# Optimization experiments

Hardware: AMD Instinct MI355X
Metric: run time of the kernel (lower is better)

The kernel has to match this reference:

```python
import jax, jax.numpy as jnp
import numpy as np

D_MODEL = 1024
H = 16
D_K = D_MODEL // H
NEG = -1e9


def setup_inputs() -> dict:
    key = jax.random.key(0)
    ks = jax.random.split(key, 8)
    B, S = 4, 2048
    q = jax.random.normal(ks[0], (B, S, D_MODEL), dtype=jnp.float32)
    k = jax.random.normal(ks[1], (B, S, D_MODEL), dtype=jnp.float32)
    v = jax.random.normal(ks[2], (B, S, D_MODEL), dtype=jnp.float32)
    mask = jax.random.randint(ks[3], (B, S), 0, 2, dtype=jnp.int32)
    scale = 1.0 / np.sqrt(D_MODEL)
    Wq = jax.random.normal(ks[4], (D_MODEL, D_MODEL), dtype=jnp.float32) * scale
    Wk = jax.random.normal(ks[5], (D_MODEL, D_MODEL), dtype=jnp.float32) * scale
    Wv = jax.random.normal(ks[6], (D_MODEL, D_MODEL), dtype=jnp.float32) * scale
    Wo = jax.random.normal(ks[7], (D_MODEL, D_MODEL), dtype=jnp.float32) * scale
    return {"q": q, "k": k, "v": v, "mask": mask,
            "Wq": Wq, "Wk": Wk, "Wv": Wv, "Wo": Wo}


def _split_heads(x):
    # [B,S,d_model] -> [B,H,S,d_k]
    B, S, _ = x.shape
    return x.reshape(B, S, H, D_K).transpose(0, 2, 1, 3)


def reference(q, k, v, mask, Wq, Wk, Wv, Wo):
    # Linear projections (torch Linear: x @ W.T, no bias)
    query = _split_heads(jnp.einsum('bsd,ed->bse', q, Wq))
    key_ = _split_heads(jnp.einsum('bsd,ed->bse', k, Wk))
    value = _split_heads(jnp.einsum('bsd,ed->bse', v, Wv))
    # scaled dot-product attention, manual path
    scores = jnp.einsum('bhqd,bhkd->bhqk', query, key_) / jnp.sqrt(
        jnp.asarray(D_K, dtype=query.dtype))
    m = (mask == 0)[:, None, None, :]  # [B,1,1,S]
    scores = jnp.where(m, jnp.asarray(NEG, dtype=scores.dtype), scores)
    attn = jax.nn.softmax(scores, axis=-1)
    mh = jnp.einsum('bhqk,bhkd->bhqd', attn, value)
    # merge heads -> [B,S,d_model]
    B = mh.shape[0]
    mh = mh.transpose(0, 2, 1, 3).reshape(B, -1, D_MODEL)
    return jnp.einsum('bsd,ed->bse', mh, Wo)
```

## Files before the change

### kernel.cpp

```cpp
#include <hip/hip_runtime.h>

typedef __attribute__((ext_vector_type(4))) float f32x4;
typedef __attribute__((ext_vector_type(8))) __bf16 bf16x8;
typedef __attribute__((ext_vector_type(2))) __bf16 bf16x2;

#if defined(__has_builtin)
#if __has_builtin(__builtin_amdgcn_exp2f)
#define EXP2F(x) __builtin_amdgcn_exp2f(x)
#endif
#if __has_builtin(__builtin_amdgcn_cvt_pk_bf16_f32)
#define HAVE_CVT_PK 1
#endif
#endif
#ifndef EXP2F
#define EXP2F(x) __builtin_exp2f(x)
#endif

__device__ __forceinline__ ushort f2bf(float f) {
  unsigned int u = __float_as_uint(f);
  return (ushort)((u + 0x7FFFu + ((u >> 16) & 1u)) >> 16);
}

__device__ __forceinline__ uint pack_bf16(float a, float b) {
#ifdef HAVE_CVT_PK
  bf16x2 p = __builtin_amdgcn_cvt_pk_bf16_f32(a, b);
  return __builtin_bit_cast(uint, p);
#else
  return (uint)f2bf(a) | ((uint)f2bf(b) << 16);
#endif
}

__device__ __forceinline__ void async_cp16(const void* g, void* l) {
  __builtin_amdgcn_global_load_lds(
      (const __attribute__((address_space(1))) void*)g,
      (__attribute__((address_space(3))) void*)l, 16, 0, 0);
}


__global__ __launch_bounds__(256) void cast_bf16_kernel(const float* __restrict__ in,
                                                        ushort* __restrict__ out, int n4) {
  int i = blockIdx.x * 256 + threadIdx.x;
  if (i < n4) {
    float4 f = ((const float4*)in)[i];
    uint2 o;
    o.x = pack_bf16(f.x, f.y);
    o.y = pack_bf16(f.z, f.w);
    ((uint2*)out)[i] = o;
  }
}

__global__ __launch_bounds__(256) void cast3_kernel(const float* __restrict__ q,
                                                    const float* __restrict__ k,
                                                    const float* __restrict__ v,
                                                    ushort* qo, ushort* ko, ushort* vo) {
  int y = blockIdx.y;
  const float* in = y == 0 ? q : (y == 1 ? k : v);
  ushort* out = y == 0 ? qo : (y == 1 ? ko : vo);
  int i = blockIdx.x * 256 + threadIdx.x;
  float4 f = ((const float4*)in)[i];
  uint2 o;
  o.x = pack_bf16(f.x, f.y);
  o.y = pack_bf16(f.z, f.w);
  ((uint2*)out)[i] = o;
}

__global__ __launch_bounds__(256) void cast4_kernel(const float* __restrict__ a,
                                                    const float* __restrict__ b,
                                                    const float* __restrict__ c,
                                                    const float* __restrict__ d,
                                                    ushort* ao, ushort* bo, ushort* co, ushort* do_) {
  int y = blockIdx.y;
  const float* in = y == 0 ? a : (y == 1 ? b : (y == 2 ? c : d));
  ushort* out = y == 0 ? ao : (y == 1 ? bo : (y == 2 ? co : do_));
  int i = blockIdx.x * 256 + threadIdx.x;
  float4 f = ((const float4*)in)[i];
  uint2 o;
  o.x = pack_bf16(f.x, f.y);
  o.y = pack_bf16(f.z, f.w);
  ((uint2*)out)[i] = o;
}


__device__ __forceinline__ void gemm_body(const ushort* __restrict__ A,
                                          const ushort* __restrict__ W,
                                          void* __restrict__ Cout, int mode) {
  constexpr int N = 1024, K = 1024;
  __shared__ ushort As[128 * 32];
  __shared__ ushort Bs[128 * 32];
  const int bm = blockIdx.y * 128;
  const int bn = blockIdx.x * 128;
  const int tid = threadIdx.x;
  const int w = tid >> 6, lane = tid & 63;
  const int g = lane >> 4, cc = lane & 15;
  const int wm = (w >> 1) * 64, wn = (w & 1) * 64;

  f32x4 acc[4][4];
#pragma unroll
  for (int i = 0; i < 4; ++i)
#pragma unroll
    for (int j = 0; j < 4; ++j) acc[i][j] = (f32x4)0.0f;

  for (int k0 = 0; k0 < K; k0 += 32) {
#pragma unroll
    for (int j = 0; j < 2; ++j) {
      int cbase = w * 128 + j * 64;
      int cid = cbase + lane;
      int row = cid & 127, kb = cid >> 7;
      async_cp16(A + (size_t)(bm + row) * K + k0 + kb * 8, &As[cbase * 8]);
      async_cp16(W + (size_t)(bn + row) * K + k0 + kb * 8, &Bs[cbase * 8]);
    }
    __syncthreads();
    bf16x8 af[4], bfr[4];
#pragma unroll
    for (int mi = 0; mi < 4; ++mi)
      af[mi] = *(const bf16x8*)&As[(g * 128 + wm + mi * 16 + cc) * 8];
#pragma unroll
    for (int ni = 0; ni < 4; ++ni)
      bfr[ni] = *(const bf16x8*)&Bs[(g * 128 + wn + ni * 16 + cc) * 8];
#pragma unroll
    for (int mi = 0; mi < 4; ++mi)
#pragma unroll
      for (int ni = 0; ni < 4; ++ni)
        acc[mi][ni] = __builtin_amdgcn_mfma_f32_16x16x32_bf16(af[mi], bfr[ni], acc[mi][ni], 0, 0, 0);
    __syncthreads();
  }

#pragma unroll
  for (int mi = 0; mi < 4; ++mi) {
#pragma unroll
    for (int ni = 0; ni < 4; ++ni) {
#pragma unroll
      for (int r = 0; r < 4; ++r) {
        int row = bm + wm + mi * 16 + g * 4 + r;
        int col = bn + wn + ni * 16 + cc;
        float val = acc[mi][ni][r];
        if (mode == 0) {
          ((ushort*)Cout)[(size_t)row * N + col] = f2bf(val);
        } else if (mode == 1) {
          ((float*)Cout)[(size_t)row * N + col] = val;
        } else {
          int b = row >> 11, s = row & 2047;
          int h = col >> 6, d = col & 63;
          ((ushort*)Cout)[(size_t)((b * 16 + h) * 64 + d) * 2048 + s] = f2bf(val);
        }
      }
    }
  }
}

__global__ __launch_bounds__(256) void qkv_gemm_kernel(const ushort* qb, const ushort* kb,
                                                       const ushort* vb, const ushort* wq,
                                                       const ushort* wk, const ushort* wv,
                                                       ushort* Qp, ushort* Kp, ushort* Vt) {
  int z = blockIdx.z;
  const ushort* A = z == 0 ? qb : (z == 1 ? kb : vb);
  const ushort* W = z == 0 ? wq : (z == 1 ? wk : wv);
  void* C = z == 0 ? (void*)Qp : (z == 1 ? (void*)Kp : (void*)Vt);
  gemm_body(A, W, C, z == 2 ? 2 : 0);
}

__global__ __launch_bounds__(256) void gemm1_kernel(const ushort* A, const ushort* W,
                                                    void* C, int mode) {
  gemm_body(A, W, C, mode);
}

__global__ __launch_bounds__(256, 4) void attn_kernel(const ushort* __restrict__ Qp,
                                                      const ushort* __restrict__ Kp,
                                                      const ushort* __restrict__ Vt,
                                                      const int* __restrict__ mask,
                                                      ushort* __restrict__ mh) {
  constexpr int S = 2048, DM = 1024, DK = 64;
  __shared__ ushort k_lds[64 * 64];
  __shared__ ushort v_lds[64 * 64];
  __shared__ ushort pt_lds[4 * 2176];

  const int bh = blockIdx.x;
  const int qt = blockIdx.y;
  const int b = bh >> 4, h = bh & 15;
  const int tid = threadIdx.x;
  const int w = tid >> 6, lane = tid & 63;
  const int g = lane >> 4, cc = lane & 15;
  ushort* ptw = &pt_lds[w * 2176];

  const int q0 = qt * 128 + w * 32;
  bf16x8 qf[2][2];
#pragma unroll
  for (int ni = 0; ni < 2; ++ni) {
    size_t row = (size_t)(b * S + q0 + ni * 16 + cc);
#pragma unroll
    for (int ks = 0; ks < 2; ++ks)
      qf[ks][ni] = *(const bf16x8*)&Qp[row * DM + h * DK + ks * 32 + g * 8];
  }

  f32x4 o_acc[4][2];
#pragma unroll
  for (int i = 0; i < 4; ++i)
#pragma unroll
    for (int j = 0; j < 2; ++j) o_acc[i][j] = (f32x4)0.0f;
  float m_i[2] = {-3e38f, -3e38f};
  float l_p[2] = {0.0f, 0.0f};
  const int* maskb = mask + b * S;
  const float csc = 0.18033688011112042f;

  for (int kt = 0; kt < S / 64; ++kt) {
    if (kt) __syncthreads();
#pragma unroll
    for (int j = 0; j < 2; ++j) {
      int cb = j * 256 + w * 64;
      int cid = cb + lane;
      async_cp16(Kp + (size_t)(b * S + kt * 64 + (cid & 63)) * DM + h * DK + (cid >> 6) * 8,
                 &k_lds[cb * 8]);
      async_cp16(Vt + (size_t)(bh * DK + (cid & 63)) * S + kt * 64 + (cid >> 6) * 8,
                 &v_lds[cb * 8]);
    }
    __syncthreads();

    f32x4 sacc[4][2];
#pragma unroll
    for (int mi = 0; mi < 4; ++mi)
#pragma unroll
      for (int ni = 0; ni < 2; ++ni) sacc[mi][ni] = (f32x4)0.0f;
#pragma unroll
    for (int ks = 0; ks < 2; ++ks)
#pragma unroll
      for (int mi = 0; mi < 4; ++mi) {
        bf16x8 kf = *(const bf16x8*)&k_lds[((ks * 4 + g) * 64 + mi * 16 + cc) * 8];
        sacc[mi][0] = __builtin_amdgcn_mfma_f32_16x16x32_bf16(kf, qf[ks][0], sacc[mi][0], 0, 0, 0);
        sacc[mi][1] = __builtin_amdgcn_mfma_f32_16x16x32_bf16(kf, qf[ks][1], sacc[mi][1], 0, 0, 0);
      }

    float mx[2] = {-3e38f, -3e38f};
#pragma unroll
    for (int mi = 0; mi < 4; ++mi) {
      int4 mv = *(const int4*)&maskb[kt * 64 + mi * 16 + g * 4];
      const int* mvp = &mv.x;
#pragma unroll
      for (int r = 0; r < 4; ++r) {
        bool keep = mvp[r] != 0;
#pragma unroll
        for (int ni = 0; ni < 2; ++ni) {
          float t = sacc[mi][ni][r] * csc;
          t = keep ? t : -1e9f;
          sacc[mi][ni][r] = t;
          mx[ni] = fmaxf(mx[ni], t);
        }
      }
    }
    float mn[2];
#pragma unroll
    for (int ni = 0; ni < 2; ++ni) {
      float m = mx[ni];
      m = fmaxf(m, __shfl_xor(m, 16, 64));
      m = fmaxf(m, __shfl_xor(m, 32, 64));
      mn[ni] = fmaxf(m_i[ni], m);
      float al = EXP2F(m_i[ni] - mn[ni]);
      m_i[ni] = mn[ni];
      l_p[ni] *= al;
#pragma unroll
      for (int md = 0; md < 4; ++md)
#pragma unroll
        for (int r = 0; r < 4; ++r) o_acc[md][ni][r] *= al;
    }

#pragma unroll
    for (int mi = 0; mi < 4; ++mi)
#pragma unroll
      for (int ni = 0; ni < 2; ++ni) {
        float p0 = EXP2F(sacc[mi][ni][0] - mn[ni]);
        float p1 = EXP2F(sacc[mi][ni][1] - mn[ni]);
        float p2 = EXP2F(sacc[mi][ni][2] - mn[ni]);
        float p3 = EXP2F(sacc[mi][ni][3] - mn[ni]);
        l_p[ni] += (p0 + p1) + (p2 + p3);
        int base = ((mi * 2 + (g >> 1)) * 32 + ni * 16 + cc) * 8 + (g & 1) * 4;
        *(uint*)&ptw[base] = pack_bf16(p0, p1);
        *(uint*)&ptw[base + 2] = pack_bf16(p2, p3);
      }

#pragma unroll
    for (int ks = 0; ks < 2; ++ks) {
      bf16x8 ptf[2];
#pragma unroll
      for (int ni = 0; ni < 2; ++ni)
        ptf[ni] = *(const bf16x8*)&ptw[((ks * 4 + g) * 32 + ni * 16 + cc) * 8];
#pragma unroll
      for (int md = 0; md < 4; ++md) {
        bf16x8 vf = *(const bf16x8*)&v_lds[((ks * 4 + g) * 64 + md * 16 + cc) * 8];
        o_acc[md][0] = __builtin_amdgcn_mfma_f32_16x16x32_bf16(vf, ptf[0], o_acc[md][0], 0, 0, 0);
        o_acc[md][1] = __builtin_amdgcn_mfma_f32_16x16x32_bf16(vf, ptf[1], o_acc[md][1], 0, 0, 0);
      }
    }
  }

  float rl[2];
#pragma unroll
  for (int ni = 0; ni < 2; ++ni) {
    float l = l_p[ni];
    l += __shfl_xor(l, 16, 64);
    l += __shfl_xor(l, 32, 64);
    rl[ni] = 1.0f / l;
  }
#pragma unroll
  for (int md = 0; md < 4; ++md)
#pragma unroll
    for (int ni = 0; ni < 2; ++ni) {
      int ql = ni * 16 + cc;
      int dbase = md * 16 + g * 4;
      *(uint*)&ptw[ql * 68 + dbase] =
          pack_bf16(o_acc[md][ni][0] * rl[ni], o_acc[md][ni][1] * rl[ni]);
      *(uint*)&ptw[ql * 68 + dbase + 2] =
          pack_bf16(o_acc[md][ni][2] * rl[ni], o_acc[md][ni][3] * rl[ni]);
    }
#pragma unroll
  for (int pass = 0; pass < 4; ++pass) {
    int ql = pass * 8 + (lane >> 3);
    int dc = lane & 7;
    uint4 val = *(const uint4*)&ptw[ql * 68 + dc * 8];
    *(uint4*)&mh[(size_t)(b * S + q0 + ql) * DM + h * DK + dc * 8] = val;
  }
}


extern "C" void kernel_launch(void* const* d_in, const int* in_sizes, int n_in,
                              void* d_out, int out_size, void* d_ws, size_t ws_size,
                              hipStream_t stream) {
  const float* q = (const float*)d_in[0];
  const float* k = (const float*)d_in[1];
  const float* v = (const float*)d_in[2];
  const int* mask = (const int*)d_in[3];
  const float* Wq = (const float*)d_in[4];
  const float* Wk = (const float*)d_in[5];
  const float* Wv = (const float*)d_in[6];
  const float* Wo = (const float*)d_in[7];

  const int M = 8192, Dm = 1024;
  const size_t MB = 1 << 20;

  char* ws = (char*)d_ws;
  ushort* Qp = (ushort*)(ws);
  ushort* Kp = (ushort*)(ws + 16 * MB);
  ushort* Vt = (ushort*)(ws + 32 * MB);
  ushort* wqb = (ushort*)(ws + 48 * MB);
  ushort* wkb = wqb + (1 << 20);
  ushort* wvb = wkb + (1 << 20);
  ushort* wob = wvb + (1 << 20);
  ushort* inbase = (ushort*)(ws + 56 * MB);

  dim3 blk(256);
  dim3 ggrid(Dm / 128, M / 128);

  cast4_kernel<<<dim3(1024, 4), blk, 0, stream>>>(Wq, Wk, Wv, Wo, wqb, wkb, wvb, wob);

  ushort* mh;
  if (ws_size >= 104 * MB) {
    ushort* qb = inbase;
    ushort* kb = inbase + 8 * MB;
    ushort* vb = inbase + 16 * MB;
    cast3_kernel<<<dim3(8192, 3), blk, 0, stream>>>(q, k, v, qb, kb, vb);
    qkv_gemm_kernel<<<dim3(Dm / 128, M / 128, 3), blk, 0, stream>>>(qb, kb, vb, wqb, wkb, wvb,
                                                                    Qp, Kp, Vt);
    mh = qb;
  } else {
    ushort* bufA = inbase;
    cast_bf16_kernel<<<dim3(8192), blk, 0, stream>>>(q, bufA, M * Dm / 4);
    gemm1_kernel<<<ggrid, blk, 0, stream>>>(bufA, wqb, (void*)Qp, 0);
    cast_bf16_kernel<<<dim3(8192), blk, 0, stream>>>(k, bufA, M * Dm / 4);
    gemm1_kernel<<<ggrid, blk, 0, stream>>>(bufA, wkb, (void*)Kp, 0);
    cast_bf16_kernel<<<dim3(8192), blk, 0, stream>>>(v, bufA, M * Dm / 4);
    gemm1_kernel<<<ggrid, blk, 0, stream>>>(bufA, wvb, (void*)Vt, 2);
    mh = bufA;
  }

  attn_kernel<<<dim3(64, 16), blk, 0, stream>>>(Qp, Kp, Vt, mask, mh);
  gemm1_kernel<<<ggrid, blk, 0, stream>>>(mh, wob, d_out, 1);
}
```

Measured before the change: 459.5 us.

## Fold softmax scale into Q projection, precompute mask bias, MFMA row sums

```diff
diff --git a/kernel.cpp b/kernel.cpp
--- a/kernel.cpp
+++ b/kernel.cpp
@@ -1,30 +1,32 @@
 #include <hip/hip_runtime.h>
+#include <math.h>
 
 typedef __attribute__((ext_vector_type(4))) float f32x4;
 typedef __attribute__((ext_vector_type(8))) __bf16 bf16x8;
 typedef __attribute__((ext_vector_type(2))) __bf16 bf16x2;
 
-#if defined(__has_builtin)
+#ifndef __has_builtin
+#define __has_builtin(x) 0
+#endif
+
 #if __has_builtin(__builtin_amdgcn_exp2f)
 #define EXP2F(x) __builtin_amdgcn_exp2f(x)
+#else
+#define EXP2F(x) exp2f(x)
 #endif
+
+__device__ __forceinline__ ushort f2bf(float f) {
+  return (ushort)((__float_as_uint(f) + 0x8000u) >> 16);
+}
+
+__device__ __forceinline__ uint pack_bf16(float a, float b) {
 #if __has_builtin(__builtin_amdgcn_cvt_pk_bf16_f32)
-#define HAVE_CVT_PK 1
-#endif
-#endif
-#ifndef EXP2F
-#define EXP2F(x) __builtin_exp2f(x)
-#endif
-
-__device__ __forceinline__ ushort f2bf(float f) {
-  unsigned int u = __float_as_uint(f);
-  return (ushort)((u + 0x7FFFu + ((u >> 16) & 1u)) >> 16);
-}
-
-__device__ __forceinline__ uint pack_bf16(float a, float b) {
-#ifdef HAVE_CVT_PK
   bf16x2 p = __builtin_amdgcn_cvt_pk_bf16_f32(a, b);
   return __builtin_bit_cast(uint, p);
+#elif __has_builtin(__builtin_amdgcn_perm)
+  uint au = __float_as_uint(a) + 0x8000u;
+  uint bu = __float_as_uint(b) + 0x8000u;
+  return __builtin_amdgcn_perm(bu, au, 0x07060302u);
 #else
   return (uint)f2bf(a) | ((uint)f2bf(b) << 16);
 #endif
@@ -37,16 +39,10 @@
 }
 
 
-__global__ __launch_bounds__(256) void cast_bf16_kernel(const float* __restrict__ in,
-                                                        ushort* __restrict__ out, int n4) {
+__global__ __launch_bounds__(256) void bias_kernel(const int* __restrict__ mask,
+                                                   float* __restrict__ bias) {
   int i = blockIdx.x * 256 + threadIdx.x;
-  if (i < n4) {
-    float4 f = ((const float4*)in)[i];
-    uint2 o;
-    o.x = pack_bf16(f.x, f.y);
-    o.y = pack_bf16(f.z, f.w);
-    ((uint2*)out)[i] = o;
-  }
+  bias[i] = mask[i] ? 0.0f : -1e9f;
 }
 
 __global__ __launch_bounds__(256) void cast3_kernel(const float* __restrict__ q,
@@ -125,6 +121,7 @@
     __syncthreads();
   }
 
+  const float qsc = 0.18033688011112042f;
 #pragma unroll
   for (int mi = 0; mi < 4; ++mi) {
 #pragma unroll
@@ -138,6 +135,8 @@
           ((ushort*)Cout)[(size_t)row * N + col] = f2bf(val);
         } else if (mode == 1) {
           ((float*)Cout)[(size_t)row * N + col] = val;
+        } else if (mode == 3) {
+          ((ushort*)Cout)[(size_t)row * N + col] = f2bf(val * qsc);
         } else {
           int b = row >> 11, s = row & 2047;
           int h = col >> 6, d = col & 63;
@@ -156,7 +155,7 @@
   const ushort* A = z == 0 ? qb : (z == 1 ? kb : vb);
   const ushort* W = z == 0 ? wq : (z == 1 ? wk : wv);
   void* C = z == 0 ? (void*)Qp : (z == 1 ? (void*)Kp : (void*)Vt);
-  gemm_body(A, W, C, z == 2 ? 2 : 0);
+  gemm_body(A, W, C, z == 2 ? 2 : (z == 0 ? 3 : 0));
 }
 
 __global__ __launch_bounds__(256) void gemm1_kernel(const ushort* A, const ushort* W,
@@ -167,7 +166,7 @@
 __global__ __launch_bounds__(256, 4) void attn_kernel(const ushort* __restrict__ Qp,
                                                       const ushort* __restrict__ Kp,
                                                       const ushort* __restrict__ Vt,
-                                                      const int* __restrict__ mask,
+                                                      const float* __restrict__ bias,
                                                       ushort* __restrict__ mh) {
   constexpr int S = 2048, DM = 1024, DK = 64;
   __shared__ ushort k_lds[64 * 64];
@@ -192,15 +191,18 @@
       qf[ks][ni] = *(const bf16x8*)&Qp[row * DM + h * DK + ks * 32 + g * 8];
   }
 
+  bf16x8 ones;
+#pragma unroll
+  for (int i = 0; i < 8; ++i) ones[i] = (__bf16)1.0f;
+
   f32x4 o_acc[4][2];
 #pragma unroll
   for (int i = 0; i < 4; ++i)
 #pragma unroll
     for (int j = 0; j < 2; ++j) o_acc[i][j] = (f32x4)0.0f;
+  f32x4 l_acc[2] = {(f32x4)0.0f, (f32x4)0.0f};
   float m_i[2] = {-3e38f, -3e38f};
-  float l_p[2] = {0.0f, 0.0f};
-  const int* maskb = mask + b * S;
-  const float csc = 0.18033688011112042f;
+  const float* biasb = bias + b * S;
 
   for (int kt = 0; kt < S / 64; ++kt) {
     if (kt) __syncthreads();
@@ -232,15 +234,13 @@
     float mx[2] = {-3e38f, -3e38f};
 #pragma unroll
     for (int mi = 0; mi < 4; ++mi) {
-      int4 mv = *(const int4*)&maskb[kt * 64 + mi * 16 + g * 4];
-      const int* mvp = &mv.x;
+      float4 bv = *(const float4*)&biasb[kt * 64 + mi * 16 + g * 4];
+      const float* bvp = &bv.x;
 #pragma unroll
       for (int r = 0; r < 4; ++r) {
-        bool keep = mvp[r] != 0;
 #pragma unroll
         for (int ni = 0; ni < 2; ++ni) {
-          float t = sacc[mi][ni][r] * csc;
-          t = keep ? t : -1e9f;
+          float t = sacc[mi][ni][r] + bvp[r];
           sacc[mi][ni][r] = t;
           mx[ni] = fmaxf(mx[ni], t);
         }
@@ -255,7 +255,7 @@
       mn[ni] = fmaxf(m_i[ni], m);
       float al = EXP2F(m_i[ni] - mn[ni]);
       m_i[ni] = mn[ni];
-      l_p[ni] *= al;
+      l_acc[ni][0] *= al;
 #pragma unroll
       for (int md = 0; md < 4; ++md)
 #pragma unroll
@@ -270,10 +270,11 @@
         float p1 = EXP2F(sacc[mi][ni][1] - mn[ni]);
         float p2 = EXP2F(sacc[mi][ni][2] - mn[ni]);
         float p3 = EXP2F(sacc[mi][ni][3] - mn[ni]);
-        l_p[ni] += (p0 + p1) + (p2 + p3);
+        uint2 pv;
+        pv.x = pack_bf16(p0, p1);
+        pv.y = pack_bf16(p2, p3);
         int base = ((mi * 2 + (g >> 1)) * 32 + ni * 16 + cc) * 8 + (g & 1) * 4;
-        *(uint*)&ptw[base] = pack_bf16(p0, p1);
-        *(uint*)&ptw[base + 2] = pack_bf16(p2, p3);
+        *(uint2*)&ptw[base] = pv;
       }
 
 #pragma unroll
@@ -282,6 +283,8 @@
 #pragma unroll
       for (int ni = 0; ni < 2; ++ni)
         ptf[ni] = *(const bf16x8*)&ptw[((ks * 4 + g) * 32 + ni * 16 + cc) * 8];
+      l_acc[0] = __builtin_amdgcn_mfma_f32_16x16x32_bf16(ones, ptf[0], l_acc[0], 0, 0, 0);
+      l_acc[1] = __builtin_amdgcn_mfma_f32_16x16x32_bf16(ones, ptf[1], l_acc[1], 0, 0, 0);
 #pragma unroll
       for (int md = 0; md < 4; ++md) {
         bf16x8 vf = *(const bf16x8*)&v_lds[((ks * 4 + g) * 64 + md * 16 + cc) * 8];
@@ -293,12 +296,8 @@
 
   float rl[2];
 #pragma unroll
-  for (int ni = 0; ni < 2; ++ni) {
-    float l = l_p[ni];
-    l += __shfl_xor(l, 16, 64);
-    l += __shfl_xor(l, 32, 64);
-    rl[ni] = 1.0f / l;
-  }
+  for (int ni = 0; ni < 2; ++ni) rl[ni] = 1.0f / l_acc[ni][0];
+
 #pragma unroll
   for (int md = 0; md < 4; ++md)
 #pragma unroll
@@ -343,33 +342,20 @@
   ushort* wkb = wqb + (1 << 20);
   ushort* wvb = wkb + (1 << 20);
   ushort* wob = wvb + (1 << 20);
-  ushort* inbase = (ushort*)(ws + 56 * MB);
+  float* biasbuf = (float*)(ws + 56 * MB);
+  ushort* vb = (ushort*)(ws + 57 * MB);
+  ushort* mh = vb;
+  ushort* qb = (ushort*)d_out;
+  ushort* kb = qb + (size_t)8 * 1024 * 1024;
 
   dim3 blk(256);
   dim3 ggrid(Dm / 128, M / 128);
 
   cast4_kernel<<<dim3(1024, 4), blk, 0, stream>>>(Wq, Wk, Wv, Wo, wqb, wkb, wvb, wob);
-
-  ushort* mh;
-  if (ws_size >= 104 * MB) {
-    ushort* qb = inbase;
-    ushort* kb = inbase + 8 * MB;
-    ushort* vb = inbase + 16 * MB;
-    cast3_kernel<<<dim3(8192, 3), blk, 0, stream>>>(q, k, v, qb, kb, vb);
-    qkv_gemm_kernel<<<dim3(Dm / 128, M / 128, 3), blk, 0, stream>>>(qb, kb, vb, wqb, wkb, wvb,
-                                                                    Qp, Kp, Vt);
-    mh = qb;
-  } else {
-    ushort* bufA = inbase;
-    cast_bf16_kernel<<<dim3(8192), blk, 0, stream>>>(q, bufA, M * Dm / 4);
-    gemm1_kernel<<<ggrid, blk, 0, stream>>>(bufA, wqb, (void*)Qp, 0);
-    cast_bf16_kernel<<<dim3(8192), blk, 0, stream>>>(k, bufA, M * Dm / 4);
-    gemm1_kernel<<<ggrid, blk, 0, stream>>>(bufA, wkb, (void*)Kp, 0);
-    cast_bf16_kernel<<<dim3(8192), blk, 0, stream>>>(v, bufA, M * Dm / 4);
-    gemm1_kernel<<<ggrid, blk, 0, stream>>>(bufA, wvb, (void*)Vt, 2);
-    mh = bufA;
-  }
-
-  attn_kernel<<<dim3(64, 16), blk, 0, stream>>>(Qp, Kp, Vt, mask, mh);
+  bias_kernel<<<dim3(32), blk, 0, stream>>>(mask, biasbuf);
+  cast3_kernel<<<dim3(8192, 3), blk, 0, stream>>>(q, k, v, qb, kb, vb);
+  qkv_gemm_kernel<<<dim3(Dm / 128, M / 128, 3), blk, 0, stream>>>(qb, kb, vb, wqb, wkb, wvb,
+                                                                  Qp, Kp, Vt);
+  attn_kernel<<<dim3(64, 16), blk, 0, stream>>>(Qp, Kp, Vt, biasbuf, mh);
   gemm1_kernel<<<ggrid, blk, 0, stream>>>(mh, wob, d_out, 1);
 }
```

Result: faster. 445.8 us (-3.0%).
